# Kernel optimization log

Hardware: AMD Instinct MI355X
Metric: run time of the kernel (lower is better)

Reference implementation:

```python
import jax, jax.numpy as jnp
import numpy as np

CHUNK_SIZE = 2048
EPS = 1e-12  # torch F.normalize clamps the norm at 1e-12


def _l2_normalize(x, axis):
    n = jnp.sqrt(jnp.sum(x * x, axis=axis, keepdims=True))
    return x / jnp.maximum(n, EPS)


def _nnfm_loss(F_r, F_s, chunk_size=CHUNK_SIZE):
    B, C, H_r, W_r = F_r.shape
    _, _, H_s, W_s = F_s.shape
    N_r = H_r * W_r
    N_s = H_s * W_s
    assert N_r % chunk_size == 0, "N_r must be divisible by chunk_size for this reference"
    n_chunks = N_r // chunk_size

    F_s_norm = _l2_normalize(F_s.reshape(B, C, N_s), axis=1)  # (B, C, N_s)
    F_r_flat = F_r.reshape(B, C, N_r)
    # (n_chunks, B, C, chunk) -- contiguous chunks along N_r, matching the torch loop
    chunks = F_r_flat.reshape(B, C, n_chunks, chunk_size).transpose(2, 0, 1, 3)

    def body(chunk):  # chunk: (B, C, chunk_size)
        cn = _l2_normalize(chunk, axis=1)
        sim = jnp.einsum('bcn,bcm->bnm', cn, F_s_norm)  # (B, chunk, N_s)
        # min(1 - sim) over N_s == 1 - max(sim)
        return 1.0 - jnp.max(sim, axis=2)  # (B, chunk)

    min_dists = jax.lax.map(body, chunks)  # (n_chunks, B, chunk) -- bounded memory
    return jnp.mean(min_dists)


def setup_inputs() -> dict:
    key = jax.random.key(0)
    k1, k2 = jax.random.split(key)
    F_r = jax.random.normal(k1, (1, 768, 128, 128), dtype=jnp.float32)
    F_s = jax.random.normal(k2, (1, 768, 128, 128), dtype=jnp.float32)
    return {"F_r": F_r, "F_s": F_s}


def reference(F_r, F_s):
    return _nnfm_loss(F_r, F_s)
```

## Files before the change

### kernel.cpp

```cpp
#include <hip/hip_runtime.h>
#include <cstdint>
#include <cstddef>

#define C_DIM 768
#define N_DIM 16384

typedef __attribute__((ext_vector_type(8))) short short8;
typedef __attribute__((ext_vector_type(4))) float f32x4;

__device__ __forceinline__ ushort f2bf(float f) {
    uint32_t u = __float_as_uint(f);
    uint32_t r = 0x7fffu + ((u >> 16) & 1u);
    return (ushort)((u + r) >> 16);
}

__device__ __forceinline__ void async_ld16(const void* g, void* l) {
    __builtin_amdgcn_global_load_lds(
        (__attribute__((address_space(1))) void*)g,
        (__attribute__((address_space(3))) void*)l,
        16, 0, 0);
}

__global__ __launch_bounds__(256) void norm_tr(const float* __restrict__ F0,
                                               ushort* __restrict__ T0,
                                               const float* __restrict__ F1,
                                               ushort* __restrict__ T1) {
    const float*  F = blockIdx.y ? F1 : F0;
    ushort*       T = blockIdx.y ? T1 : T0;
    const int i0 = blockIdx.x * 64;
    const int t  = threadIdx.x;
    const int tx = t & 63;
    const int ty = t >> 6;

    float ss = 0.f;
    for (int c = ty; c < C_DIM; c += 4) {
        float v = F[(size_t)c * N_DIM + i0 + tx];
        ss += v * v;
    }
    __shared__ float red[4][64];
    __shared__ float scale[64];
    red[ty][tx] = ss;
    __syncthreads();
    if (t < 64) {
        float s = red[0][t] + red[1][t] + red[2][t] + red[3][t];
        float n = sqrtf(s);
        scale[t] = 1.0f / fmaxf(n, 1e-12f);
    }
    __syncthreads();

    __shared__ float tile[64][65];
    const int i_l   = t >> 3;
    const int c_off = (t & 7) * 8;
    for (int c0 = 0; c0 < C_DIM; c0 += 64) {
        #pragma unroll
        for (int rr = 0; rr < 16; ++rr) {
            int c_l = rr * 4 + ty;
            tile[c_l][tx] = F[(size_t)(c0 + c_l) * N_DIM + i0 + tx] * scale[tx];
        }
        __syncthreads();
        #pragma unroll
        for (int half = 0; half < 2; ++half) {
            int il = i_l + half * 32;
            __align__(16) ushort pack[8];
            #pragma unroll
            for (int j = 0; j < 8; ++j)
                pack[j] = f2bf(tile[c_off + j][il]);
            *(uint4*)&T[(size_t)(i0 + il) * C_DIM + c0 + c_off] = *(const uint4*)pack;
        }
        __syncthreads();
    }
}

__global__ __launch_bounds__(512) void gemm_rowmax(const ushort* __restrict__ A,
                                                   const ushort* __restrict__ B,
                                                   unsigned* __restrict__ rowkey) {
    __shared__ __align__(16) ushort As[2][128 * 32];
    __shared__ __align__(16) ushort Bs[2][256 * 32];

    const int t    = threadIdx.x;
    const int lane = t & 63;
    const int w    = t >> 6;
    const int wm   = w >> 2;
    const int wn   = w & 3;

    const int bid   = blockIdx.x;
    const int xcd   = bid & 7;
    const int local = bid >> 3;
    const int m0    = (local >> 3) * 128;
    const int n0    = (xcd * 8 + (local & 7)) * 256;

    f32x4 acc[4][4];
    #pragma unroll
    for (int i = 0; i < 4; ++i)
        #pragma unroll
        for (int j = 0; j < 4; ++j)
            acc[i][j] = (f32x4){0.f, 0.f, 0.f, 0.f};

    const int kq = ((t & 3) ^ ((t >> 3) & 3)) * 8;
    const ushort* ag  = A + (size_t)(m0 + (t >> 2)) * C_DIM + kq;
    const ushort* bg0 = B + (size_t)(n0 + (t >> 2)) * C_DIM + kq;
    const ushort* bg1 = bg0 + (size_t)128 * C_DIM;
    const int lda = t * 8;
    const int ldb0 = t * 8, ldb1 = 128 * 32 + t * 8;

    const int qp    = ((lane >> 4) ^ ((lane >> 1) & 3)) * 8;
    const int a_off = (wm * 64 + (lane & 15)) * 32 + qp;
    const int b_off = (wn * 64 + (lane & 15)) * 32 + qp;

    async_ld16(ag,  As[0] + lda);
    async_ld16(bg0, Bs[0] + ldb0);
    async_ld16(bg1, Bs[0] + ldb1);

    int buf = 0;
    for (int k0 = 0; k0 < C_DIM - 32; k0 += 32) {
        const int kn = k0 + 32, nb = buf ^ 1;
        async_ld16(ag + kn,  As[nb] + lda);
        async_ld16(bg0 + kn, Bs[nb] + ldb0);
        async_ld16(bg1 + kn, Bs[nb] + ldb1);

        asm volatile("s_waitcnt vmcnt(3)" ::: "memory");
        __builtin_amdgcn_s_barrier();

        const ushort* Ab = As[buf];
        const ushort* Bb = Bs[buf];
        short8 af[4], bfr[4];
        #pragma unroll
        for (int mt = 0; mt < 4; ++mt)
            af[mt] = *(const short8*)(Ab + a_off + mt * 16 * 32);
        #pragma unroll
        for (int nt = 0; nt < 4; ++nt)
            bfr[nt] = *(const short8*)(Bb + b_off + nt * 16 * 32);

        __builtin_amdgcn_s_setprio(1);
        #pragma unroll
        for (int mt = 0; mt < 4; ++mt)
            #pragma unroll
            for (int nt = 0; nt < 4; ++nt)
                acc[mt][nt] = __builtin_amdgcn_mfma_f32_16x16x32_bf16(
                    af[mt], bfr[nt], acc[mt][nt], 0, 0, 0);
        __builtin_amdgcn_s_setprio(0);

        asm volatile("s_waitcnt lgkmcnt(0)" ::: "memory");
        __builtin_amdgcn_s_barrier();
        buf ^= 1;
    }

    {
        asm volatile("s_waitcnt vmcnt(0)" ::: "memory");
        __builtin_amdgcn_s_barrier();
        const ushort* Ab = As[buf];
        const ushort* Bb = Bs[buf];
        short8 af[4], bfr[4];
        #pragma unroll
        for (int mt = 0; mt < 4; ++mt)
            af[mt] = *(const short8*)(Ab + a_off + mt * 16 * 32);
        #pragma unroll
        for (int nt = 0; nt < 4; ++nt)
            bfr[nt] = *(const short8*)(Bb + b_off + nt * 16 * 32);
        __builtin_amdgcn_s_setprio(1);
        #pragma unroll
        for (int mt = 0; mt < 4; ++mt)
            #pragma unroll
            for (int nt = 0; nt < 4; ++nt)
                acc[mt][nt] = __builtin_amdgcn_mfma_f32_16x16x32_bf16(
                    af[mt], bfr[nt], acc[mt][nt], 0, 0, 0);
        __builtin_amdgcn_s_setprio(0);
    }

    #pragma unroll
    for (int mt = 0; mt < 4; ++mt) {
        #pragma unroll
        for (int reg = 0; reg < 4; ++reg) {
            float v = fmaxf(fmaxf(acc[mt][0][reg], acc[mt][1][reg]),
                            fmaxf(acc[mt][2][reg], acc[mt][3][reg]));
            #pragma unroll
            for (int off = 1; off < 16; off <<= 1)
                v = fmaxf(v, __shfl_xor(v, off, 64));
            if ((lane & 15) == 0) {
                int m = m0 + wm * 64 + mt * 16 + (lane >> 4) * 4 + reg;
                unsigned u = __float_as_uint(v);
                u = (u & 0x80000000u) ? ~u : (u | 0x80000000u);
                atomicMax(&rowkey[m], u);
            }
        }
    }
}

__global__ __launch_bounds__(1024) void finalize(const unsigned* __restrict__ rowkey,
                                                 float* __restrict__ out) {
    const int t = threadIdx.x;
    float s = 0.f;
    for (int i = t; i < N_DIM; i += 1024) {
        unsigned u = rowkey[i];
        float f = (u & 0x80000000u) ? __uint_as_float(u ^ 0x80000000u)
                                    : __uint_as_float(~u);
        s += f;
    }
    #pragma unroll
    for (int off = 32; off >= 1; off >>= 1)
        s += __shfl_down(s, off, 64);
    __shared__ float part[16];
    if ((t & 63) == 0) part[t >> 6] = s;
    __syncthreads();
    if (t == 0) {
        float tot = 0.f;
        #pragma unroll
        for (int i = 0; i < 16; ++i) tot += part[i];
        out[0] = 1.0f - tot * (1.0f / (float)N_DIM);
    }
}

extern "C" void kernel_launch(void* const* d_in, const int* in_sizes, int n_in,
                              void* d_out, int out_size, void* d_ws, size_t ws_size,
                              hipStream_t stream) {
    const float* F_r = (const float*)d_in[0];
    const float* F_s = (const float*)d_in[1];

    ushort*   Rt     = (ushort*)d_ws;
    ushort*   St     = Rt + (size_t)N_DIM * C_DIM;
    unsigned* rowkey = (unsigned*)(St + (size_t)N_DIM * C_DIM);
    float*    out    = (float*)d_out;

    hipLaunchKernelGGL(norm_tr, dim3(N_DIM / 64, 2), dim3(256), 0, stream,
                       F_r, Rt, F_s, St);
    hipMemsetAsync(rowkey, 0, N_DIM * sizeof(unsigned), stream);
    hipLaunchKernelGGL(gemm_rowmax, dim3((N_DIM / 128) * (N_DIM / 256)), dim3(512),
                       0, stream, Rt, St, rowkey);
    hipLaunchKernelGGL(finalize, dim3(1), dim3(1024), 0, stream, rowkey, out);
}
```

Before: 711.1 us.

## Enlarge GEMM tile to 256x256 with K=64 stages and interleaved quadrant pipeline

The row-max GEMM moves from 128x256 tiles with K=32 double buffering to 256x256 tiles with K=64 stages, so each wave computes a 128x64 sub-tile with an 8x4 accumulator array. Each stage is split into four MFMA quadrants, and async global-to-LDS loads for the next stage are issued into quadrant buffers as soon as they are freed. This raises arithmetic intensity per loaded byte, halves the grid size, and overlaps loads with compute. In exchange it uses more registers and tighter barrier and vmcnt bookkeeping, which could limit occupancy or introduce hazards.

```diff
diff --git a/kernel.cpp b/kernel.cpp
--- a/kernel.cpp
+++ b/kernel.cpp
@@ -19,6 +19,12 @@
         (__attribute__((address_space(1))) void*)g,
         (__attribute__((address_space(3))) void*)l,
         16, 0, 0);
+}
+
+template<int N> __device__ __forceinline__ void wait_vmcnt() {
+    if constexpr (N == 4)      asm volatile("s_waitcnt vmcnt(4)" ::: "memory");
+    else if constexpr (N == 2) asm volatile("s_waitcnt vmcnt(2)" ::: "memory");
+    else if constexpr (N == 0) asm volatile("s_waitcnt vmcnt(0)" ::: "memory");
 }
 
 __global__ __launch_bounds__(256) void norm_tr(const float* __restrict__ F0,
@@ -71,11 +77,118 @@
     }
 }
 
-__global__ __launch_bounds__(512) void gemm_rowmax(const ushort* __restrict__ A,
-                                                   const ushort* __restrict__ B,
-                                                   unsigned* __restrict__ rowkey) {
-    __shared__ __align__(16) ushort As[2][128 * 32];
-    __shared__ __align__(16) ushort Bs[2][256 * 32];
+__device__ __forceinline__ f32x4 mfma16(short8 a, short8 b, f32x4 c) {
+    return __builtin_amdgcn_mfma_f32_16x16x32_bf16(a, b, c, 0, 0, 0);
+}
+
+template<bool STAGE, int W0, int W1, int W3>
+__device__ __forceinline__ void half_iter(
+    ushort* As, ushort* Bs,
+    const ushort* agA, const ushort* bgB,
+    int ktn,
+    int ldst, int abase, int bbase, int aq0, int aq1,
+    f32x4 (&acc)[8][4])
+{
+    const int ko = ktn * 64;
+    short8 a03[4][2], a47[4][2], b01[2][2], b23[2][2];
+
+    #pragma unroll
+    for (int mt = 0; mt < 4; ++mt) {
+        a03[mt][0] = *(const short8*)(As + abase + mt * 1024 + aq0);
+        a03[mt][1] = *(const short8*)(As + abase + mt * 1024 + aq1);
+    }
+    #pragma unroll
+    for (int nt = 0; nt < 2; ++nt) {
+        b01[nt][0] = *(const short8*)(Bs + bbase + nt * 1024 + aq0);
+        b01[nt][1] = *(const short8*)(Bs + bbase + nt * 1024 + aq1);
+    }
+    __builtin_amdgcn_s_barrier();
+    asm volatile("s_waitcnt lgkmcnt(0)" ::: "memory");
+    __builtin_amdgcn_sched_barrier(0);
+    __builtin_amdgcn_s_setprio(1);
+    #pragma unroll
+    for (int mt = 0; mt < 4; ++mt)
+        #pragma unroll
+        for (int nt = 0; nt < 2; ++nt) {
+            acc[mt][nt] = mfma16(a03[mt][0], b01[nt][0], acc[mt][nt]);
+            acc[mt][nt] = mfma16(a03[mt][1], b01[nt][1], acc[mt][nt]);
+        }
+    __builtin_amdgcn_s_setprio(0);
+    wait_vmcnt<W0>();
+    __builtin_amdgcn_s_barrier();
+
+    #pragma unroll
+    for (int nt = 0; nt < 2; ++nt) {
+        b23[nt][0] = *(const short8*)(Bs + 8192 + bbase + nt * 1024 + aq0);
+        b23[nt][1] = *(const short8*)(Bs + 8192 + bbase + nt * 1024 + aq1);
+    }
+    if constexpr (STAGE) {
+        async_ld16(agA + ko,                 As + ldst);
+        async_ld16(agA + ko + 128 * C_DIM,   As + 8192 + ldst);
+        async_ld16(bgB + ko,                 Bs + ldst);
+        async_ld16(bgB + ko + 128 * C_DIM,   Bs + 4096 + ldst);
+    }
+    __builtin_amdgcn_s_barrier();
+    asm volatile("s_waitcnt lgkmcnt(0)" ::: "memory");
+    __builtin_amdgcn_sched_barrier(0);
+    __builtin_amdgcn_s_setprio(1);
+    #pragma unroll
+    for (int mt = 0; mt < 4; ++mt)
+        #pragma unroll
+        for (int nt = 0; nt < 2; ++nt) {
+            acc[mt][2 + nt] = mfma16(a03[mt][0], b23[nt][0], acc[mt][2 + nt]);
+            acc[mt][2 + nt] = mfma16(a03[mt][1], b23[nt][1], acc[mt][2 + nt]);
+        }
+    __builtin_amdgcn_s_setprio(0);
+    wait_vmcnt<W1>();
+    __builtin_amdgcn_s_barrier();
+
+    #pragma unroll
+    for (int mt = 0; mt < 4; ++mt) {
+        a47[mt][0] = *(const short8*)(As + 4096 + abase + mt * 1024 + aq0);
+        a47[mt][1] = *(const short8*)(As + 4096 + abase + mt * 1024 + aq1);
+    }
+    if constexpr (STAGE) {
+        async_ld16(bgB + ko + 32 * C_DIM,    Bs + 8192 + ldst);
+        async_ld16(bgB + ko + 160 * C_DIM,   Bs + 12288 + ldst);
+    }
+    __builtin_amdgcn_s_barrier();
+    asm volatile("s_waitcnt lgkmcnt(0)" ::: "memory");
+    __builtin_amdgcn_sched_barrier(0);
+    __builtin_amdgcn_s_setprio(1);
+    #pragma unroll
+    for (int mt = 0; mt < 4; ++mt)
+        #pragma unroll
+        for (int nt = 0; nt < 2; ++nt) {
+            acc[4 + mt][nt] = mfma16(a47[mt][0], b01[nt][0], acc[4 + mt][nt]);
+            acc[4 + mt][nt] = mfma16(a47[mt][1], b01[nt][1], acc[4 + mt][nt]);
+        }
+    __builtin_amdgcn_s_setprio(0);
+    __builtin_amdgcn_s_barrier();
+
+    if constexpr (STAGE) {
+        async_ld16(agA + ko + 64 * C_DIM,    As + 4096 + ldst);
+        async_ld16(agA + ko + 192 * C_DIM,   As + 12288 + ldst);
+    }
+    __builtin_amdgcn_s_barrier();
+    __builtin_amdgcn_s_setprio(1);
+    #pragma unroll
+    for (int mt = 0; mt < 4; ++mt)
+        #pragma unroll
+        for (int nt = 0; nt < 2; ++nt) {
+            acc[4 + mt][2 + nt] = mfma16(a47[mt][0], b23[nt][0], acc[4 + mt][2 + nt]);
+            acc[4 + mt][2 + nt] = mfma16(a47[mt][1], b23[nt][1], acc[4 + mt][2 + nt]);
+        }
+    __builtin_amdgcn_s_setprio(0);
+    wait_vmcnt<W3>();
+    __builtin_amdgcn_s_barrier();
+}
+
+__global__ __launch_bounds__(512, 2) void gemm_rowmax(const ushort* __restrict__ A,
+                                                      const ushort* __restrict__ B,
+                                                      unsigned* __restrict__ rowkey) {
+    __shared__ __align__(16) ushort As[16384];
+    __shared__ __align__(16) ushort Bs[16384];
 
     const int t    = threadIdx.x;
     const int lane = t & 63;
@@ -86,89 +199,48 @@
     const int bid   = blockIdx.x;
     const int xcd   = bid & 7;
     const int local = bid >> 3;
-    const int m0    = (local >> 3) * 128;
+    const int m0    = (local >> 3) * 256;
     const int n0    = (xcd * 8 + (local & 7)) * 256;
 
-    f32x4 acc[4][4];
-    #pragma unroll
-    for (int i = 0; i < 4; ++i)
+    f32x4 acc[8][4];
+    #pragma unroll
+    for (int i = 0; i < 8; ++i)
         #pragma unroll
         for (int j = 0; j < 4; ++j)
             acc[i][j] = (f32x4){0.f, 0.f, 0.f, 0.f};
 
-    const int kq = ((t & 3) ^ ((t >> 3) & 3)) * 8;
-    const ushort* ag  = A + (size_t)(m0 + (t >> 2)) * C_DIM + kq;
-    const ushort* bg0 = B + (size_t)(n0 + (t >> 2)) * C_DIM + kq;
-    const ushort* bg1 = bg0 + (size_t)128 * C_DIM;
-    const int lda = t * 8;
-    const int ldb0 = t * 8, ldb1 = 128 * 32 + t * 8;
-
-    const int qp    = ((lane >> 4) ^ ((lane >> 1) & 3)) * 8;
-    const int a_off = (wm * 64 + (lane & 15)) * 32 + qp;
-    const int b_off = (wn * 64 + (lane & 15)) * 32 + qp;
-
-    async_ld16(ag,  As[0] + lda);
-    async_ld16(bg0, Bs[0] + ldb0);
-    async_ld16(bg1, Bs[0] + ldb1);
-
-    int buf = 0;
-    for (int k0 = 0; k0 < C_DIM - 32; k0 += 32) {
-        const int kn = k0 + 32, nb = buf ^ 1;
-        async_ld16(ag + kn,  As[nb] + lda);
-        async_ld16(bg0 + kn, Bs[nb] + ldb0);
-        async_ld16(bg1 + kn, Bs[nb] + ldb1);
-
-        asm volatile("s_waitcnt vmcnt(3)" ::: "memory");
-        __builtin_amdgcn_s_barrier();
-
-        const ushort* Ab = As[buf];
-        const ushort* Bb = Bs[buf];
-        short8 af[4], bfr[4];
-        #pragma unroll
-        for (int mt = 0; mt < 4; ++mt)
-            af[mt] = *(const short8*)(Ab + a_off + mt * 16 * 32);
-        #pragma unroll
-        for (int nt = 0; nt < 4; ++nt)
-            bfr[nt] = *(const short8*)(Bb + b_off + nt * 16 * 32);
-
-        __builtin_amdgcn_s_setprio(1);
-        #pragma unroll
-        for (int mt = 0; mt < 4; ++mt)
-            #pragma unroll
-            for (int nt = 0; nt < 4; ++nt)
-                acc[mt][nt] = __builtin_amdgcn_mfma_f32_16x16x32_bf16(
-                    af[mt], bfr[nt], acc[mt][nt], 0, 0, 0);
-        __builtin_amdgcn_s_setprio(0);
-
-        asm volatile("s_waitcnt lgkmcnt(0)" ::: "memory");
-        __builtin_amdgcn_s_barrier();
-        buf ^= 1;
-    }
-
-    {
-        asm volatile("s_waitcnt vmcnt(0)" ::: "memory");
-        __builtin_amdgcn_s_barrier();
-        const ushort* Ab = As[buf];
-        const ushort* Bb = Bs[buf];
-        short8 af[4], bfr[4];
-        #pragma unroll
-        for (int mt = 0; mt < 4; ++mt)
-            af[mt] = *(const short8*)(Ab + a_off + mt * 16 * 32);
-        #pragma unroll
-        for (int nt = 0; nt < 4; ++nt)
-            bfr[nt] = *(const short8*)(Bb + b_off + nt * 16 * 32);
-        __builtin_amdgcn_s_setprio(1);
-        #pragma unroll
-        for (int mt = 0; mt < 4; ++mt)
-            #pragma unroll
-            for (int nt = 0; nt < 4; ++nt)
-                acc[mt][nt] = __builtin_amdgcn_mfma_f32_16x16x32_bf16(
-                    af[mt], bfr[nt], acc[mt][nt], 0, 0, 0);
-        __builtin_amdgcn_s_setprio(0);
-    }
-
-    #pragma unroll
-    for (int mt = 0; mt < 4; ++mt) {
+    const int srow = t >> 3;
+    const int schk = ((t & 7) ^ (srow & 7)) * 8;
+    const ushort* agA = A + (size_t)(m0 + srow) * C_DIM + schk;
+    const int brow = ((t >> 8) & 1) * 64 + (srow & 31);
+    const ushort* bgB = B + (size_t)(n0 + brow) * C_DIM + schk;
+    const int ldst = t * 8;
+
+    const int aq0   = ((lane >> 4) ^ (lane & 7)) * 8;
+    const int aq1   = (((lane >> 4) + 4) ^ (lane & 7)) * 8;
+    const int abase = wm * 8192 + (lane & 15) * 64;
+    const int bbase = wn * 2048 + (lane & 15) * 64;
+
+    async_ld16(agA,                 As + ldst);
+    async_ld16(agA + 128 * C_DIM,   As + 8192 + ldst);
+    async_ld16(bgB,                 Bs + ldst);
+    async_ld16(bgB + 128 * C_DIM,   Bs + 4096 + ldst);
+    async_ld16(bgB + 32 * C_DIM,    Bs + 8192 + ldst);
+    async_ld16(bgB + 160 * C_DIM,   Bs + 12288 + ldst);
+    async_ld16(agA + 64 * C_DIM,    As + 4096 + ldst);
+    async_ld16(agA + 192 * C_DIM,   As + 12288 + ldst);
+    wait_vmcnt<4>();
+    __builtin_amdgcn_s_barrier();
+
+    #pragma unroll 1
+    for (int j = 0; j < 11; ++j)
+        half_iter<true, 2, 4, 4>(As, Bs, agA, bgB, j + 1,
+                                 ldst, abase, bbase, aq0, aq1, acc);
+    half_iter<false, 2, 0, -1>(As, Bs, agA, bgB, 0,
+                               ldst, abase, bbase, aq0, aq1, acc);
+
+    #pragma unroll
+    for (int mt = 0; mt < 8; ++mt) {
         #pragma unroll
         for (int reg = 0; reg < 4; ++reg) {
             float v = fmaxf(fmaxf(acc[mt][0][reg], acc[mt][1][reg]),
@@ -177,7 +249,7 @@
             for (int off = 1; off < 16; off <<= 1)
                 v = fmaxf(v, __shfl_xor(v, off, 64));
             if ((lane & 15) == 0) {
-                int m = m0 + wm * 64 + mt * 16 + (lane >> 4) * 4 + reg;
+                int m = m0 + wm * 128 + mt * 16 + (lane >> 4) * 4 + reg;
                 unsigned u = __float_as_uint(v);
                 u = (u & 0x80000000u) ? ~u : (u | 0x80000000u);
                 atomicMax(&rowkey[m], u);
@@ -224,7 +296,7 @@
     hipLaunchKernelGGL(norm_tr, dim3(N_DIM / 64, 2), dim3(256), 0, stream,
                        F_r, Rt, F_s, St);
     hipMemsetAsync(rowkey, 0, N_DIM * sizeof(unsigned), stream);
-    hipLaunchKernelGGL(gemm_rowmax, dim3((N_DIM / 128) * (N_DIM / 256)), dim3(512),
+    hipLaunchKernelGGL(gemm_rowmax, dim3((N_DIM / 256) * (N_DIM / 256)), dim3(512),
                        0, stream, Rt, St, rowkey);
     hipLaunchKernelGGL(finalize, dim3(1), dim3(1024), 0, stream, rowkey, out);
 }
```

Result: slower. 820.8 us (+15.4%).

## Add 256x256-tile GEMM with 8-phase ping-pong LDS pipeline and XOR swizzle

Applied to the files above, without the earlier changes.

Adds a new GEMM+rowmax kernel that uses 256x256 output tiles with a K-step of 64, held in 128 KB of dynamic LDS as double buffers. Each K-step is split into eight phases, each interleaving register fragment loads, asynchronous global-to-LDS prefetch of sub-tiles and a block of MFMAs, with barriers and priority hints between phases. The larger tile doubles MFMA work per byte loaded from global memory and halves the number of rowmax atomics per row. In exchange it uses much more LDS and registers, limiting blocks per CU and adding sync points. The old 128x256 kernel stays as a fallback if the large LDS allocation is not allowed.

```diff
diff --git a/kernel.cpp b/kernel.cpp
--- a/kernel.cpp
+++ b/kernel.cpp
@@ -19,6 +19,10 @@
         (__attribute__((address_space(1))) void*)g,
         (__attribute__((address_space(3))) void*)l,
         16, 0, 0);
+}
+
+__device__ __forceinline__ f32x4 mfma16(short8 a, short8 b, f32x4 c) {
+    return __builtin_amdgcn_mfma_f32_16x16x32_bf16(a, b, c, 0, 0, 0);
 }
 
 __global__ __launch_bounds__(256) void norm_tr(const float* __restrict__ F0,
@@ -71,9 +75,265 @@
     }
 }
 
-__global__ __launch_bounds__(512) void gemm_rowmax(const ushort* __restrict__ A,
-                                                   const ushort* __restrict__ B,
-                                                   unsigned* __restrict__ rowkey) {
+template<int N> __device__ __forceinline__ void wait_vmcnt() {
+    if constexpr (N == 6)      asm volatile("s_waitcnt vmcnt(6)" ::: "memory");
+    else if constexpr (N == 0) asm volatile("s_waitcnt vmcnt(0)" ::: "memory");
+}
+
+__device__ __forceinline__ void phase_head() {
+    __builtin_amdgcn_s_barrier();
+    asm volatile("s_waitcnt lgkmcnt(0)" ::: "memory");
+    __builtin_amdgcn_sched_barrier(0);
+    __builtin_amdgcn_s_setprio(1);
+}
+
+__device__ __forceinline__ void st_r0(const ushort* agA, int ko, ushort* Aw, int ldst) {
+    async_ld16(agA + ko,                 Aw + ldst);
+    async_ld16(agA + ko + 128 * C_DIM,   Aw + 8192 + ldst);
+}
+__device__ __forceinline__ void st_r1(const ushort* agA, int ko, ushort* Aw, int ldst) {
+    async_ld16(agA + ko + 64 * C_DIM,    Aw + 4096 + ldst);
+    async_ld16(agA + ko + 192 * C_DIM,   Aw + 12288 + ldst);
+}
+__device__ __forceinline__ void st_s0(const ushort* bgB, int ko, ushort* Bw, int ldst) {
+    async_ld16(bgB + ko,                 Bw + ldst);
+    async_ld16(bgB + ko + 128 * C_DIM,   Bw + 4096 + ldst);
+}
+__device__ __forceinline__ void st_s1(const ushort* bgB, int ko, ushort* Bw, int ldst) {
+    async_ld16(bgB + ko + 32 * C_DIM,    Bw + 8192 + ldst);
+    async_ld16(bgB + ko + 160 * C_DIM,   Bw + 12288 + ldst);
+}
+
+template<bool TAIL>
+__device__ __forceinline__ void big_iter(
+    ushort* Ae, ushort* Be, ushort* Ao, ushort* Bo,
+    const ushort* agA, const ushort* bgB,
+    int kO, int kE2, int kO2,
+    int ldst, int abase, int bbase, int aq0, int aq1,
+    short8 (&a03)[4][2], short8 (&a47)[4][2],
+    short8 (&b01)[2][2], short8 (&b23)[2][2],
+    f32x4 (&acc)[8][4])
+{
+    #pragma unroll
+    for (int mt = 0; mt < 4; ++mt) {
+        a03[mt][0] = *(const short8*)(Ae + abase + mt * 1024 + aq0);
+        a03[mt][1] = *(const short8*)(Ae + abase + mt * 1024 + aq1);
+    }
+    #pragma unroll
+    for (int nt = 0; nt < 2; ++nt) {
+        b01[nt][0] = *(const short8*)(Be + bbase + nt * 1024 + aq0);
+        b01[nt][1] = *(const short8*)(Be + bbase + nt * 1024 + aq1);
+    }
+    st_r1(agA, kO, Ao, ldst);
+    phase_head();
+    #pragma unroll
+    for (int mt = 0; mt < 4; ++mt)
+        #pragma unroll
+        for (int nt = 0; nt < 2; ++nt) {
+            acc[mt][nt] = mfma16(a03[mt][0], b01[nt][0], acc[mt][nt]);
+            acc[mt][nt] = mfma16(a03[mt][1], b01[nt][1], acc[mt][nt]);
+        }
+    __builtin_amdgcn_s_setprio(0);
+    __builtin_amdgcn_s_barrier();
+
+    #pragma unroll
+    for (int nt = 0; nt < 2; ++nt) {
+        b23[nt][0] = *(const short8*)(Be + 8192 + bbase + nt * 1024 + aq0);
+        b23[nt][1] = *(const short8*)(Be + 8192 + bbase + nt * 1024 + aq1);
+    }
+    if constexpr (!TAIL) st_r0(agA, kE2, Ae, ldst);
+    phase_head();
+    #pragma unroll
+    for (int mt = 0; mt < 4; ++mt)
+        #pragma unroll
+        for (int nt = 0; nt < 2; ++nt) {
+            acc[mt][2 + nt] = mfma16(a03[mt][0], b23[nt][0], acc[mt][2 + nt]);
+            acc[mt][2 + nt] = mfma16(a03[mt][1], b23[nt][1], acc[mt][2 + nt]);
+        }
+    __builtin_amdgcn_s_setprio(0);
+    __builtin_amdgcn_s_barrier();
+
+    #pragma unroll
+    for (int mt = 0; mt < 4; ++mt) {
+        a47[mt][0] = *(const short8*)(Ae + 4096 + abase + mt * 1024 + aq0);
+        a47[mt][1] = *(const short8*)(Ae + 4096 + abase + mt * 1024 + aq1);
+    }
+    if constexpr (!TAIL) st_s0(bgB, kE2, Be, ldst);
+    phase_head();
+    #pragma unroll
+    for (int mt = 0; mt < 4; ++mt)
+        #pragma unroll
+        for (int nt = 0; nt < 2; ++nt) {
+            acc[4 + mt][nt] = mfma16(a47[mt][0], b01[nt][0], acc[4 + mt][nt]);
+            acc[4 + mt][nt] = mfma16(a47[mt][1], b01[nt][1], acc[4 + mt][nt]);
+        }
+    __builtin_amdgcn_s_setprio(0);
+    __builtin_amdgcn_s_barrier();
+
+    if constexpr (!TAIL) st_s1(bgB, kE2, Be, ldst);
+    phase_head();
+    #pragma unroll
+    for (int mt = 0; mt < 4; ++mt)
+        #pragma unroll
+        for (int nt = 0; nt < 2; ++nt) {
+            acc[4 + mt][2 + nt] = mfma16(a47[mt][0], b23[nt][0], acc[4 + mt][2 + nt]);
+            acc[4 + mt][2 + nt] = mfma16(a47[mt][1], b23[nt][1], acc[4 + mt][2 + nt]);
+        }
+    __builtin_amdgcn_s_setprio(0);
+    if constexpr (!TAIL) wait_vmcnt<6>(); else wait_vmcnt<0>();
+    __builtin_amdgcn_s_barrier();
+
+    #pragma unroll
+    for (int mt = 0; mt < 4; ++mt) {
+        a03[mt][0] = *(const short8*)(Ao + abase + mt * 1024 + aq0);
+        a03[mt][1] = *(const short8*)(Ao + abase + mt * 1024 + aq1);
+    }
+    #pragma unroll
+    for (int nt = 0; nt < 2; ++nt) {
+        b01[nt][0] = *(const short8*)(Bo + bbase + nt * 1024 + aq0);
+        b01[nt][1] = *(const short8*)(Bo + bbase + nt * 1024 + aq1);
+    }
+    if constexpr (!TAIL) st_r1(agA, kE2, Ae, ldst);
+    phase_head();
+    #pragma unroll
+    for (int mt = 0; mt < 4; ++mt)
+        #pragma unroll
+        for (int nt = 0; nt < 2; ++nt) {
+            acc[mt][nt] = mfma16(a03[mt][0], b01[nt][0], acc[mt][nt]);
+            acc[mt][nt] = mfma16(a03[mt][1], b01[nt][1], acc[mt][nt]);
+        }
+    __builtin_amdgcn_s_setprio(0);
+    __builtin_amdgcn_s_barrier();
+
+    #pragma unroll
+    for (int nt = 0; nt < 2; ++nt) {
+        b23[nt][0] = *(const short8*)(Bo + 8192 + bbase + nt * 1024 + aq0);
+        b23[nt][1] = *(const short8*)(Bo + 8192 + bbase + nt * 1024 + aq1);
+    }
+    if constexpr (!TAIL) st_r0(agA, kO2, Ao, ldst);
+    phase_head();
+    #pragma unroll
+    for (int mt = 0; mt < 4; ++mt)
+        #pragma unroll
+        for (int nt = 0; nt < 2; ++nt) {
+            acc[mt][2 + nt] = mfma16(a03[mt][0], b23[nt][0], acc[mt][2 + nt]);
+            acc[mt][2 + nt] = mfma16(a03[mt][1], b23[nt][1], acc[mt][2 + nt]);
+        }
+    __builtin_amdgcn_s_setprio(0);
+    __builtin_amdgcn_s_barrier();
+
+    #pragma unroll
+    for (int mt = 0; mt < 4; ++mt) {
+        a47[mt][0] = *(const short8*)(Ao + 4096 + abase + mt * 1024 + aq0);
+        a47[mt][1] = *(const short8*)(Ao + 4096 + abase + mt * 1024 + aq1);
+    }
+    if constexpr (!TAIL) st_s0(bgB, kO2, Bo, ldst);
+    phase_head();
+    #pragma unroll
+    for (int mt = 0; mt < 4; ++mt)
+        #pragma unroll
+        for (int nt = 0; nt < 2; ++nt) {
+            acc[4 + mt][nt] = mfma16(a47[mt][0], b01[nt][0], acc[4 + mt][nt]);
+            acc[4 + mt][nt] = mfma16(a47[mt][1], b01[nt][1], acc[4 + mt][nt]);
+        }
+    __builtin_amdgcn_s_setprio(0);
+    __builtin_amdgcn_s_barrier();
+
+    if constexpr (!TAIL) st_s1(bgB, kO2, Bo, ldst);
+    phase_head();
+    #pragma unroll
+    for (int mt = 0; mt < 4; ++mt)
+        #pragma unroll
+        for (int nt = 0; nt < 2; ++nt) {
+            acc[4 + mt][2 + nt] = mfma16(a47[mt][0], b23[nt][0], acc[4 + mt][2 + nt]);
+            acc[4 + mt][2 + nt] = mfma16(a47[mt][1], b23[nt][1], acc[4 + mt][2 + nt]);
+        }
+    __builtin_amdgcn_s_setprio(0);
+    if constexpr (!TAIL) wait_vmcnt<6>();
+    __builtin_amdgcn_s_barrier();
+}
+
+__global__ __launch_bounds__(512, 2) void gemm_rowmax_big(const ushort* __restrict__ A,
+                                                          const ushort* __restrict__ B,
+                                                          unsigned* __restrict__ rowkey) {
+    extern __shared__ __align__(16) ushort lds[];
+    ushort* Ae = lds;
+    ushort* Ao = lds + 16384;
+    ushort* Be = lds + 32768;
+    ushort* Bo = lds + 49152;
+
+    const int t    = threadIdx.x;
+    const int lane = t & 63;
+    const int w    = t >> 6;
+    const int wm   = w >> 2;
+    const int wn   = w & 3;
+
+    const int bid   = blockIdx.x;
+    const int xcd   = bid & 7;
+    const int local = bid >> 3;
+    const int m0    = (local >> 3) * 256;
+    const int n0    = (xcd * 8 + (local & 7)) * 256;
+
+    f32x4 acc[8][4];
+    #pragma unroll
+    for (int i = 0; i < 8; ++i)
+        #pragma unroll
+        for (int j = 0; j < 4; ++j)
+            acc[i][j] = (f32x4){0.f, 0.f, 0.f, 0.f};
+
+    const int srow = t >> 3;
+    const int schk = ((t & 7) ^ (srow & 7)) * 8;
+    const ushort* agA = A + (size_t)(m0 + srow) * C_DIM + schk;
+    const int brow = ((t >> 8) & 1) * 64 + (srow & 31);
+    const ushort* bgB = B + (size_t)(n0 + brow) * C_DIM + schk;
+    const int ldst = t * 8;
+
+    const int aq0   = ((lane >> 4) ^ (lane & 7)) * 8;
+    const int aq1   = (((lane >> 4) + 4) ^ (lane & 7)) * 8;
+    const int abase = wm * 8192 + (lane & 15) * 64;
+    const int bbase = wn * 2048 + (lane & 15) * 64;
+
+    short8 a03[4][2], a47[4][2], b01[2][2], b23[2][2];
+
+    st_r0(agA, 0, Ae, ldst);  st_s0(bgB, 0, Be, ldst);
+    st_s1(bgB, 0, Be, ldst);  st_r1(agA, 0, Ae, ldst);
+    st_r0(agA, 64, Ao, ldst); st_s0(bgB, 64, Bo, ldst); st_s1(bgB, 64, Bo, ldst);
+    wait_vmcnt<6>();
+    __builtin_amdgcn_s_barrier();
+
+    #pragma unroll 1
+    for (int j = 0; j < 5; ++j)
+        big_iter<false>(Ae, Be, Ao, Bo, agA, bgB,
+                        (2 * j + 1) * 64, (2 * j + 2) * 64, (2 * j + 3) * 64,
+                        ldst, abase, bbase, aq0, aq1,
+                        a03, a47, b01, b23, acc);
+    big_iter<true>(Ae, Be, Ao, Bo, agA, bgB,
+                   11 * 64, 0, 0,
+                   ldst, abase, bbase, aq0, aq1,
+                   a03, a47, b01, b23, acc);
+
+    #pragma unroll
+    for (int mt = 0; mt < 8; ++mt) {
+        #pragma unroll
+        for (int reg = 0; reg < 4; ++reg) {
+            float v = fmaxf(fmaxf(acc[mt][0][reg], acc[mt][1][reg]),
+                            fmaxf(acc[mt][2][reg], acc[mt][3][reg]));
+            #pragma unroll
+            for (int off = 1; off < 16; off <<= 1)
+                v = fmaxf(v, __shfl_xor(v, off, 64));
+            if ((lane & 15) == 0) {
+                int m = m0 + wm * 128 + mt * 16 + (lane >> 4) * 4 + reg;
+                unsigned u = __float_as_uint(v);
+                u = (u & 0x80000000u) ? ~u : (u | 0x80000000u);
+                atomicMax(&rowkey[m], u);
+            }
+        }
+    }
+}
+
+__global__ __launch_bounds__(512) void gemm_rowmax_fb(const ushort* __restrict__ A,
+                                                      const ushort* __restrict__ B,
+                                                      unsigned* __restrict__ rowkey) {
     __shared__ __align__(16) ushort As[2][128 * 32];
     __shared__ __align__(16) ushort Bs[2][256 * 32];
 
@@ -136,15 +396,13 @@
         for (int mt = 0; mt < 4; ++mt)
             #pragma unroll
             for (int nt = 0; nt < 4; ++nt)
-                acc[mt][nt] = __builtin_amdgcn_mfma_f32_16x16x32_bf16(
-                    af[mt], bfr[nt], acc[mt][nt], 0, 0, 0);
+                acc[mt][nt] = mfma16(af[mt], bfr[nt], acc[mt][nt]);
         __builtin_amdgcn_s_setprio(0);
 
         asm volatile("s_waitcnt lgkmcnt(0)" ::: "memory");
         __builtin_amdgcn_s_barrier();
         buf ^= 1;
     }
-
     {
         asm volatile("s_waitcnt vmcnt(0)" ::: "memory");
         __builtin_amdgcn_s_barrier();
@@ -162,8 +420,7 @@
         for (int mt = 0; mt < 4; ++mt)
             #pragma unroll
             for (int nt = 0; nt < 4; ++nt)
-                acc[mt][nt] = __builtin_amdgcn_mfma_f32_16x16x32_bf16(
-                    af[mt], bfr[nt], acc[mt][nt], 0, 0, 0);
+                acc[mt][nt] = mfma16(af[mt], bfr[nt], acc[mt][nt]);
         __builtin_amdgcn_s_setprio(0);
     }
 
@@ -221,10 +478,31 @@
     unsigned* rowkey = (unsigned*)(St + (size_t)N_DIM * C_DIM);
     float*    out    = (float*)d_out;
 
+    static int big_ok = -1;
+    if (big_ok < 0) {
+        (void)hipFuncSetAttribute((const void*)gemm_rowmax_big,
+                                  hipFuncAttributeMaxDynamicSharedMemorySize,
+                                  131072);
+        hipFuncAttributes fa{};
+        int ok = 0;
+        if (hipFuncGetAttributes(&fa, (const void*)gemm_rowmax_big) == hipSuccess &&
+            fa.maxDynamicSharedSizeBytes >= 131072)
+            ok = 1;
+        (void)hipGetLastError();
+        big_ok = ok;
+    }
+
     hipLaunchKernelGGL(norm_tr, dim3(N_DIM / 64, 2), dim3(256), 0, stream,
                        F_r, Rt, F_s, St);
     hipMemsetAsync(rowkey, 0, N_DIM * sizeof(unsigned), stream);
-    hipLaunchKernelGGL(gemm_rowmax, dim3((N_DIM / 128) * (N_DIM / 256)), dim3(512),
-                       0, stream, Rt, St, rowkey);
+    if (big_ok) {
+        hipLaunchKernelGGL(gemm_rowmax_big,
+                           dim3((N_DIM / 256) * (N_DIM / 256)), dim3(512),
+                           131072, stream, Rt, St, rowkey);
+    } else {
+        hipLaunchKernelGGL(gemm_rowmax_fb,
+                           dim3((N_DIM / 128) * (N_DIM / 256)), dim3(512),
+                           0, stream, Rt, St, rowkey);
+    }
     hipLaunchKernelGGL(finalize, dim3(1), dim3(1024), 0, stream, rowkey, out);
 }
```

Result: slower. 741.5 us (+4.3%).
